# Performance work log

Hardware: AMD Instinct MI355X
Metric: run time of the kernel (lower is better)

The kernel has to match this reference:

```python
import jax, jax.numpy as jnp
import numpy as np

KY = KX = 3  # kernel_size
PAD_Y = (KY - 1) // 2
PAD_X = (KX - 1) // 2


def setup_inputs() -> dict:
    key = jax.random.key(0)
    x = jax.random.uniform(key, (8, 3, 512, 512), dtype=jnp.float32)
    return {"x": x}


def reference(x) -> jnp.ndarray:
    # Median blur: zero-pad, gather the KYxKX neighborhood per pixel,
    # take the (lower) median along the window axis, matching
    # torch's conv2d(one-hot)+median(dim=2)[0].
    b, c, h, w = x.shape
    xp = jnp.pad(x, ((0, 0), (0, 0), (PAD_Y, PAD_Y), (PAD_X, PAD_X)))
    # (B, C, KY*KX, H, W) -- same intermediate layout as the torch im2col
    patches = jnp.stack(
        [xp[:, :, i:i + h, j:j + w] for i in range(KY) for j in range(KX)],
        axis=2,
    )
    n = KY * KX
    s = jnp.sort(patches, axis=2)
    # torch.median returns the lower median (index (n-1)//2 of sorted values)
    return s[:, :, (n - 1) // 2]
```

## Files before the change

kernel.cpp:

```cpp
#include <hip/hip_runtime.h>


#define MB_W 512
#define MB_H 512
#define MB_PLANES (8 * 3)
#define MB_STRIPS (MB_H / 4)
#define MB_XQ (MB_W / 4)
#define MB_THREADS (MB_PLANES * MB_STRIPS * MB_XQ)

__device__ __forceinline__ float min3f(float a, float b, float c) {
    return fminf(fminf(a, b), c);
}
__device__ __forceinline__ float max3f(float a, float b, float c) {
    return fmaxf(fmaxf(a, b), c);
}
__device__ __forceinline__ float med3f(float a, float b, float c) {
    return __builtin_amdgcn_fmed3f(a, b, c);
}

__global__ __launch_bounds__(256) void median_blur_kernel(
        const float* __restrict__ in, float* __restrict__ out) {
    const int gid  = blockIdx.x * blockDim.x + threadIdx.x;
    const int xq   = gid & (MB_XQ - 1);
    const int sg   = gid >> 7;
    const int y0   = (sg & (MB_STRIPS - 1)) << 2;
    const int pl   = sg >> 7;
    const int x0   = xq << 2;

    const float* pb = in + (size_t)pl * (MB_H * MB_W);

    float a[6][6];
    #pragma unroll
    for (int dy = 0; dy < 6; ++dy) {
        const int yy = y0 + dy - 1;
        if (yy >= 0 && yy < MB_H) {
            const float* rp = pb + (size_t)yy * MB_W;
            const float4 v = *reinterpret_cast<const float4*>(rp + x0);
            a[dy][1] = v.x; a[dy][2] = v.y; a[dy][3] = v.z; a[dy][4] = v.w;
            a[dy][0] = (x0 > 0)        ? rp[x0 - 1] : 0.0f;
            a[dy][5] = (x0 + 4 < MB_W) ? rp[x0 + 4] : 0.0f;
        } else {
            #pragma unroll
            for (int k = 0; k < 6; ++k) a[dy][k] = 0.0f;
        }
    }

    float* ob = out + (size_t)pl * (MB_H * MB_W) + (size_t)y0 * MB_W + x0;
    #pragma unroll
    for (int w = 0; w < 4; ++w) {
        float lo[6], mi[6], hi[6];
        #pragma unroll
        for (int k = 0; k < 6; ++k) {
            lo[k] = min3f(a[w][k], a[w + 1][k], a[w + 2][k]);
            mi[k] = med3f(a[w][k], a[w + 1][k], a[w + 2][k]);
            hi[k] = max3f(a[w][k], a[w + 1][k], a[w + 2][k]);
        }
        float4 o;
        float r[4];
        #pragma unroll
        for (int j = 0; j < 4; ++j) {
            const float A = max3f(lo[j], lo[j + 1], lo[j + 2]);
            const float B = med3f(mi[j], mi[j + 1], mi[j + 2]);
            const float C = min3f(hi[j], hi[j + 1], hi[j + 2]);
            r[j] = med3f(A, B, C);
        }
        o.x = r[0]; o.y = r[1]; o.z = r[2]; o.w = r[3];
        *reinterpret_cast<float4*>(ob + (size_t)w * MB_W) = o;
    }
}

extern "C" void kernel_launch(void* const* d_in, const int* in_sizes, int n_in,
                              void* d_out, int out_size, void* d_ws, size_t ws_size,
                              hipStream_t stream) {
    const float* x = (const float*)d_in[0];
    float* out = (float*)d_out;
    const int threads = 256;
    const int blocks = MB_THREADS / threads;
    median_blur_kernel<<<blocks, threads, 0, stream>>>(x, out);
}
```

Before: 76.41 us.

## Widen per-thread tile to 8 columns and fetch halo columns via wavefront shuffles

Each thread now handles an 8x4 output tile, so one 64-lane wavefront covers a full 512-wide row strip. The left and right halo columns come from neighbouring lanes through shuffles instead of extra scalar global loads, and columns shared between adjacent pixels are reused more within a thread. This removes the two unaligned scalar loads per row and halves thread count, at the cost of more registers per thread; launch bounds now request 3 blocks per CU.

Result: no change. 76.39 us (-0.0%).

```diff
diff --git a/kernel.cpp b/kernel.cpp
--- a/kernel.cpp
+++ b/kernel.cpp
@@ -5,8 +5,7 @@
 #define MB_H 512
 #define MB_PLANES (8 * 3)
 #define MB_STRIPS (MB_H / 4)
-#define MB_XQ (MB_W / 4)
-#define MB_THREADS (MB_PLANES * MB_STRIPS * MB_XQ)
+#define MB_THREADS (MB_PLANES * MB_STRIPS * 64)
 
 __device__ __forceinline__ float min3f(float a, float b, float c) {
     return fminf(fminf(a, b), c);
@@ -18,54 +17,73 @@
     return __builtin_amdgcn_fmed3f(a, b, c);
 }
 
-__global__ __launch_bounds__(256) void median_blur_kernel(
+__global__ __launch_bounds__(256, 3) void median_blur_kernel(
         const float* __restrict__ in, float* __restrict__ out) {
     const int gid  = blockIdx.x * blockDim.x + threadIdx.x;
-    const int xq   = gid & (MB_XQ - 1);
-    const int sg   = gid >> 7;
+    const int lane = gid & 63;
+    const int sg   = gid >> 6;
     const int y0   = (sg & (MB_STRIPS - 1)) << 2;
     const int pl   = sg >> 7;
-    const int x0   = xq << 2;
+    const int x0   = lane << 3;
 
     const float* pb = in + (size_t)pl * (MB_H * MB_W);
 
-    float a[6][6];
+    float b[6][8];
     #pragma unroll
     for (int dy = 0; dy < 6; ++dy) {
         const int yy = y0 + dy - 1;
         if (yy >= 0 && yy < MB_H) {
-            const float* rp = pb + (size_t)yy * MB_W;
-            const float4 v = *reinterpret_cast<const float4*>(rp + x0);
-            a[dy][1] = v.x; a[dy][2] = v.y; a[dy][3] = v.z; a[dy][4] = v.w;
-            a[dy][0] = (x0 > 0)        ? rp[x0 - 1] : 0.0f;
-            a[dy][5] = (x0 + 4 < MB_W) ? rp[x0 + 4] : 0.0f;
+            const float* rp = pb + (size_t)yy * MB_W + x0;
+            const float4 v0 = *reinterpret_cast<const float4*>(rp);
+            const float4 v1 = *reinterpret_cast<const float4*>(rp + 4);
+            b[dy][0] = v0.x; b[dy][1] = v0.y; b[dy][2] = v0.z; b[dy][3] = v0.w;
+            b[dy][4] = v1.x; b[dy][5] = v1.y; b[dy][6] = v1.z; b[dy][7] = v1.w;
         } else {
             #pragma unroll
-            for (int k = 0; k < 6; ++k) a[dy][k] = 0.0f;
+            for (int k = 0; k < 8; ++k) b[dy][k] = 0.0f;
         }
+    }
+
+    float hl[6], hr[6];
+    #pragma unroll
+    for (int dy = 0; dy < 6; ++dy) {
+        const float l = __shfl_up(b[dy][7], 1);
+        const float r = __shfl_down(b[dy][0], 1);
+        hl[dy] = (lane == 0)  ? 0.0f : l;
+        hr[dy] = (lane == 63) ? 0.0f : r;
     }
 
     float* ob = out + (size_t)pl * (MB_H * MB_W) + (size_t)y0 * MB_W + x0;
     #pragma unroll
     for (int w = 0; w < 4; ++w) {
-        float lo[6], mi[6], hi[6];
+        float lo[10], mi[10], hi[10];
+        lo[0] = min3f(hl[w], hl[w + 1], hl[w + 2]);
+        mi[0] = med3f(hl[w], hl[w + 1], hl[w + 2]);
+        hi[0] = max3f(hl[w], hl[w + 1], hl[w + 2]);
         #pragma unroll
-        for (int k = 0; k < 6; ++k) {
-            lo[k] = min3f(a[w][k], a[w + 1][k], a[w + 2][k]);
-            mi[k] = med3f(a[w][k], a[w + 1][k], a[w + 2][k]);
-            hi[k] = max3f(a[w][k], a[w + 1][k], a[w + 2][k]);
+        for (int k = 0; k < 8; ++k) {
+            lo[k + 1] = min3f(b[w][k], b[w + 1][k], b[w + 2][k]);
+            mi[k + 1] = med3f(b[w][k], b[w + 1][k], b[w + 2][k]);
+            hi[k + 1] = max3f(b[w][k], b[w + 1][k], b[w + 2][k]);
         }
-        float4 o;
-        float r[4];
+        lo[9] = min3f(hr[w], hr[w + 1], hr[w + 2]);
+        mi[9] = med3f(hr[w], hr[w + 1], hr[w + 2]);
+        hi[9] = max3f(hr[w], hr[w + 1], hr[w + 2]);
+
+        float r[8];
         #pragma unroll
-        for (int j = 0; j < 4; ++j) {
+        for (int j = 0; j < 8; ++j) {
             const float A = max3f(lo[j], lo[j + 1], lo[j + 2]);
             const float B = med3f(mi[j], mi[j + 1], mi[j + 2]);
             const float C = min3f(hi[j], hi[j + 1], hi[j + 2]);
             r[j] = med3f(A, B, C);
         }
-        o.x = r[0]; o.y = r[1]; o.z = r[2]; o.w = r[3];
-        *reinterpret_cast<float4*>(ob + (size_t)w * MB_W) = o;
+        float4 o0, o1;
+        o0.x = r[0]; o0.y = r[1]; o0.z = r[2]; o0.w = r[3];
+        o1.x = r[4]; o1.y = r[5]; o1.z = r[6]; o1.w = r[7];
+        float* op = ob + (size_t)w * MB_W;
+        *reinterpret_cast<float4*>(op)     = o0;
+        *reinterpret_cast<float4*>(op + 4) = o1;
     }
 }
 
```
